# Kernel tuning notes

Hardware: AMD Instinct MI355X
Metric: run time of the kernel (lower is better)

Reference implementation:

```python
import jax, jax.numpy as jnp
import numpy as np

N = 50000
E = 800000
IN_C, HID, OUT_C = 128, 64, 64
L = 8
ALPHA, THETA = 0.1, 0.5


def setup_inputs() -> dict:
    key = jax.random.key(0)
    ks = jax.random.split(key, 7)
    x = jax.random.normal(ks[0], (N, IN_C), dtype=jnp.float32)
    edge_index = jax.random.randint(ks[1], (2, E), 0, N, dtype=jnp.int64)
    # parameters (Linear weights stored [out, in] like torch)
    w_in = jax.random.normal(ks[2], (HID, IN_C), dtype=jnp.float32) / np.sqrt(IN_C)
    b_in = jnp.zeros((HID,), dtype=jnp.float32)
    conv_w = jax.random.normal(ks[3], (L, HID, HID), dtype=jnp.float32) / np.sqrt(HID)
    w_out = jax.random.normal(ks[4], (OUT_C, HID), dtype=jnp.float32) / np.sqrt(HID)
    b_out = jnp.zeros((OUT_C,), dtype=jnp.float32)
    return {"x": x, "edge_index": edge_index, "w_in": w_in, "b_in": b_in,
            "conv_w": conv_w, "w_out": w_out, "b_out": b_out}


def reference(x, edge_index, w_in, b_in, conv_w, w_out, b_out):
    # add self loops
    loops = jnp.arange(N, dtype=edge_index.dtype)
    row = jnp.concatenate([edge_index[0], loops])
    col = jnp.concatenate([edge_index[1], loops])
    # symmetric GCN normalization from in-degree of col
    deg = jax.ops.segment_sum(jnp.ones_like(col, dtype=x.dtype), col, num_segments=N)
    dinv = jnp.where(deg > 0, jax.lax.rsqrt(deg), 0.0)
    norm = (dinv[row] * dinv[col])[:, None]  # [E+N, 1]

    # eval mode: dropout is identity
    h = jax.nn.relu(x @ w_in.T + b_in)
    x0 = h
    betas = jnp.log(THETA / jnp.arange(1, L + 1, dtype=jnp.float32) + 1.0)

    def layer(h, wb):
        W, beta = wb
        agg = jax.ops.segment_sum(h[row] * norm, col, num_segments=N)  # gather-scale-scatter
        agg = (1.0 - ALPHA) * agg + ALPHA * x0                         # initial residual
        out = (1.0 - beta) * agg + beta * (agg @ W.T)                  # identity mapping
        return jax.nn.relu(out), None

    h, _ = jax.lax.scan(layer, h, (conv_w, betas))
    return h @ w_out.T + b_out
```

## Files before the change

### kernel.cpp

```cpp
#include <hip/hip_runtime.h>
#include <math.h>

#define NN 50000
#define EE 800000
#define INC 128
#define HIDC 64
#define OUTC 64
#define LLAYERS 8
#define TOT (EE + NN)
#define NB 196
#define ABLK 256
#define CHUNKA ((TOT + ABLK - 1) / ABLK)

#define WAVE_LDS_FENCE() asm volatile("s_waitcnt lgkmcnt(0)" ::: "memory")

typedef __attribute__((ext_vector_type(8))) short bf16x8;
typedef __attribute__((ext_vector_type(4))) float f32x4;

__device__ __forceinline__ float bf2f(unsigned short u) {
    return __uint_as_float(((unsigned int)u) << 16);
}
__device__ __forceinline__ unsigned short f2bf(float f) {
    unsigned int u = __float_as_uint(f);
    u += 0x7FFFu + ((u >> 16) & 1u);
    return (unsigned short)(u >> 16);
}

__global__ void detect_kernel(const long long* __restrict__ p, int* __restrict__ flag) {
    long long v = p[threadIdx.x];
    if (v < 0 || v >= NN) atomicOr(flag, 1);
}

__device__ __forceinline__ int load_row(const void* ei, int is64, int e) {
    return is64 ? (int)((const long long*)ei)[e] : ((const int*)ei)[e];
}
__device__ __forceinline__ int load_col(const void* ei, int is64, int e) {
    return is64 ? (int)((const long long*)ei)[EE + e] : ((const int*)ei)[EE + e];
}

__global__ __launch_bounds__(256) void histA(const void* __restrict__ ei,
                                             const int* __restrict__ flag,
                                             int* __restrict__ bcnt) {
    __shared__ int h[NB];
    int tid = threadIdx.x;
    for (int i = tid; i < NB; i += 256) h[i] = 0;
    __syncthreads();
    int is64 = (*flag == 0);
    int lo = blockIdx.x * CHUNKA, hi = lo + CHUNKA; if (hi > TOT) hi = TOT;
    for (int e = lo + tid; e < hi; e += 256) {
        int c = (e < EE) ? load_col(ei, is64, e) : (e - EE);
        atomicAdd(&h[c >> 8], 1);
    }
    __syncthreads();
    for (int i = tid; i < NB; i += 256) if (h[i]) atomicAdd(&bcnt[i], h[i]);
}

__global__ __launch_bounds__(256) void scan_buckets(const int* __restrict__ bcnt,
                                                    int* __restrict__ bstart,
                                                    int* __restrict__ bcur) {
    __shared__ int s[256];
    int t = threadIdx.x;
    int v = (t < NB) ? bcnt[t] : 0;
    s[t] = v;
    __syncthreads();
    for (int off = 1; off < 256; off <<= 1) {
        int a = (t >= off) ? s[t - off] : 0;
        __syncthreads();
        s[t] += a;
        __syncthreads();
    }
    if (t < NB) { int st = s[t] - v; bstart[t] = st; bcur[t] = st; }
    if (t == NB - 1) bstart[NB] = s[t];
}

__global__ __launch_bounds__(256) void bucket_scatter(const void* __restrict__ ei,
                                                      const int* __restrict__ flag,
                                                      int* __restrict__ bcur,
                                                      unsigned int* __restrict__ barr) {
    __shared__ int h[NB];
    __shared__ int base[NB];
    int tid = threadIdx.x;
    for (int i = tid; i < NB; i += 256) h[i] = 0;
    __syncthreads();
    int is64 = (*flag == 0);
    int lo = blockIdx.x * CHUNKA, hi = lo + CHUNKA; if (hi > TOT) hi = TOT;
    for (int e = lo + tid; e < hi; e += 256) {
        int c = (e < EE) ? load_col(ei, is64, e) : (e - EE);
        atomicAdd(&h[c >> 8], 1);
    }
    __syncthreads();
    for (int i = tid; i < NB; i += 256) {
        int cnt = h[i];
        base[i] = cnt ? atomicAdd(&bcur[i], cnt) : 0;
        h[i] = 0;
    }
    __syncthreads();
    for (int e = lo + tid; e < hi; e += 256) {
        int r, c;
        if (e < EE) { r = load_row(ei, is64, e); c = load_col(ei, is64, e); }
        else        { r = e - EE; c = r; }
        int b = c >> 8;
        int p = base[b] + atomicAdd(&h[b], 1);
        barr[p] = ((unsigned int)r << 8) | (unsigned int)(c & 255);
    }
}

__global__ __launch_bounds__(256) void bucket_offsets(const unsigned int* __restrict__ barr,
                                                      const int* __restrict__ bstart,
                                                      int* __restrict__ offsets,
                                                      float* __restrict__ dinv) {
    __shared__ int cnt[256];
    __shared__ int pre[256];
    int b = blockIdx.x, t = threadIdx.x;
    cnt[t] = 0;
    __syncthreads();
    int lo = bstart[b], hi = bstart[b + 1];
    for (int i = lo + t; i < hi; i += 256) atomicAdd(&cnt[barr[i] & 255u], 1);
    __syncthreads();
    int v = cnt[t];
    pre[t] = v;
    __syncthreads();
    for (int off = 1; off < 256; off <<= 1) {
        int a = (t >= off) ? pre[t - off] : 0;
        __syncthreads();
        pre[t] += a;
        __syncthreads();
    }
    int c = (b << 8) + t;
    if (c <= NN) offsets[c] = bstart[b] + pre[t] - v;
    if (c < NN)  dinv[c] = 1.0f / sqrtf((float)v);
}

__global__ __launch_bounds__(256) void bucket_place(const unsigned int* __restrict__ barr,
                                                    const int* __restrict__ bstart,
                                                    const int* __restrict__ offsets,
                                                    const float* __restrict__ dinv,
                                                    int2* __restrict__ adj) {
    __shared__ int cur[256];
    int b = blockIdx.x, t = threadIdx.x;
    int c0 = b << 8;
    int c = c0 + t;
    cur[t] = (c < NN) ? offsets[c] : 0;
    __syncthreads();
    int lo = bstart[b], hi = bstart[b + 1];
    for (int i = lo + t; i < hi; i += 256) {
        unsigned int v = barr[i];
        int r = (int)(v >> 8);
        int ci = (int)(v & 255u);
        int pos = atomicAdd(&cur[ci], 1);
        adj[pos] = make_int2(r, __float_as_int(dinv[r] * dinv[c0 + ci]));
    }
}

__global__ __launch_bounds__(256) void in_gemm(const float* __restrict__ x,
                                               const float* __restrict__ w_in,
                                               const float* __restrict__ b_in,
                                               unsigned short* __restrict__ h,
                                               float* __restrict__ x0) {
    __shared__ unsigned short xT[16 * 136];
    int tid = threadIdx.x, w = tid >> 6, lane = tid & 63;
    int g = lane >> 4, c = lane & 15;
    int base = blockIdx.x << 4;

    bf16x8 bfrag[4];
    {
        const float* Wrow = w_in + (size_t)((w << 4) + c) * INC;
        #pragma unroll
        for (int kt = 0; kt < 4; ++kt) {
            int k0 = kt * 32 + (g << 3);
            float4 va = *reinterpret_cast<const float4*>(Wrow + k0);
            float4 vb = *reinterpret_cast<const float4*>(Wrow + k0 + 4);
            bf16x8 r;
            r[0] = (short)f2bf(va.x); r[1] = (short)f2bf(va.y);
            r[2] = (short)f2bf(va.z); r[3] = (short)f2bf(va.w);
            r[4] = (short)f2bf(vb.x); r[5] = (short)f2bf(vb.y);
            r[6] = (short)f2bf(vb.z); r[7] = (short)f2bf(vb.w);
            bfrag[kt] = r;
        }
    }

    #pragma unroll
    for (int m = 0; m < 2; ++m) {
        int idx = tid * 2 + m;
        int row = idx >> 5, col4 = idx & 31;
        float4 v = *reinterpret_cast<const float4*>(
            x + (((size_t)(base + row)) << 7) + (col4 << 2));
        ushort4 pk;
        pk.x = f2bf(v.x); pk.y = f2bf(v.y); pk.z = f2bf(v.z); pk.w = f2bf(v.w);
        *reinterpret_cast<ushort4*>(&xT[row * 136 + (col4 << 2)]) = pk;
    }
    __syncthreads();

    f32x4 d = {0.f, 0.f, 0.f, 0.f};
    #pragma unroll
    for (int kt = 0; kt < 4; ++kt) {
        bf16x8 a = *reinterpret_cast<const bf16x8*>(&xT[c * 136 + kt * 32 + (g << 3)]);
        d = __builtin_amdgcn_mfma_f32_16x16x32_bf16(a, bfrag[kt], d, 0, 0, 0);
    }
    float bj = b_in[(w << 4) + c];
    #pragma unroll
    for (int r = 0; r < 4; ++r) {
        int node = base + (g << 2) + r;
        int ch = (w << 4) + c;
        float v = fmaxf(d[r] + bj, 0.0f);
        h[((size_t)node << 6) + ch]  = f2bf(v);
        x0[((size_t)node << 6) + ch] = v;
    }
}

__global__ __launch_bounds__(256) void layer_mfma(
        const unsigned short* __restrict__ h_in, unsigned short* __restrict__ h_out,
        const float* __restrict__ x0,
        const int* __restrict__ offsets, const int2* __restrict__ adj,
        const float* __restrict__ W, float beta) {
    __shared__ unsigned short aggT[16 * 72];
    int tid = threadIdx.x, w = tid >> 6, lane = tid & 63;
    int g = lane >> 4, c = lane & 15;
    float omb = 1.0f - beta;

    bf16x8 bfrag[2];
    {
        int n = (w << 4) + c;
        const float* Wrow = W + n * HIDC;
        #pragma unroll
        for (int kt = 0; kt < 2; ++kt) {
            int k0 = kt * 32 + (g << 3);
            float4 va = *reinterpret_cast<const float4*>(Wrow + k0);
            float4 vb = *reinterpret_cast<const float4*>(Wrow + k0 + 4);
            float e[8] = {va.x, va.y, va.z, va.w, vb.x, vb.y, vb.z, vb.w};
            bf16x8 r;
            #pragma unroll
            for (int i = 0; i < 8; ++i) {
                float t = beta * e[i] + ((k0 + i == n) ? omb : 0.0f);
                r[i] = (short)f2bf(t);
            }
            bfrag[kt] = r;
        }
    }

    int base = blockIdx.x << 4;
    int n = base + (w << 2) + g;
    int e0 = offsets[n], e1 = offsets[n + 1];
    float4 acc = make_float4(0.f, 0.f, 0.f, 0.f);
    int e = e0;
    for (; e + 4 <= e1; e += 4) {
        int2 a0 = adj[e], a1 = adj[e + 1], a2 = adj[e + 2], a3 = adj[e + 3];
        ushort4 h0 = *reinterpret_cast<const ushort4*>(h_in + ((a0.x << 6) + (c << 2)));
        ushort4 h1 = *reinterpret_cast<const ushort4*>(h_in + ((a1.x << 6) + (c << 2)));
        ushort4 h2 = *reinterpret_cast<const ushort4*>(h_in + ((a2.x << 6) + (c << 2)));
        ushort4 h3 = *reinterpret_cast<const ushort4*>(h_in + ((a3.x << 6) + (c << 2)));
        float n0 = __int_as_float(a0.y), n1 = __int_as_float(a1.y);
        float n2 = __int_as_float(a2.y), n3 = __int_as_float(a3.y);
        acc.x = fmaf(n0, bf2f(h0.x), acc.x); acc.y = fmaf(n0, bf2f(h0.y), acc.y);
        acc.z = fmaf(n0, bf2f(h0.z), acc.z); acc.w = fmaf(n0, bf2f(h0.w), acc.w);
        acc.x = fmaf(n1, bf2f(h1.x), acc.x); acc.y = fmaf(n1, bf2f(h1.y), acc.y);
        acc.z = fmaf(n1, bf2f(h1.z), acc.z); acc.w = fmaf(n1, bf2f(h1.w), acc.w);
        acc.x = fmaf(n2, bf2f(h2.x), acc.x); acc.y = fmaf(n2, bf2f(h2.y), acc.y);
        acc.z = fmaf(n2, bf2f(h2.z), acc.z); acc.w = fmaf(n2, bf2f(h2.w), acc.w);
        acc.x = fmaf(n3, bf2f(h3.x), acc.x); acc.y = fmaf(n3, bf2f(h3.y), acc.y);
        acc.z = fmaf(n3, bf2f(h3.z), acc.z); acc.w = fmaf(n3, bf2f(h3.w), acc.w);
    }
    for (; e < e1; ++e) {
        int2 a = adj[e];
        ushort4 hv = *reinterpret_cast<const ushort4*>(h_in + ((a.x << 6) + (c << 2)));
        float nrm = __int_as_float(a.y);
        acc.x = fmaf(nrm, bf2f(hv.x), acc.x);
        acc.y = fmaf(nrm, bf2f(hv.y), acc.y);
        acc.z = fmaf(nrm, bf2f(hv.z), acc.z);
        acc.w = fmaf(nrm, bf2f(hv.w), acc.w);
    }
    {
        const float4 x0v = *reinterpret_cast<const float4*>(x0 + ((n << 6) + (c << 2)));
        ushort4 pk;
        pk.x = f2bf(fmaf(0.9f, acc.x, 0.1f * x0v.x));
        pk.y = f2bf(fmaf(0.9f, acc.y, 0.1f * x0v.y));
        pk.z = f2bf(fmaf(0.9f, acc.z, 0.1f * x0v.z));
        pk.w = f2bf(fmaf(0.9f, acc.w, 0.1f * x0v.w));
        int row = (w << 2) + g;
        *reinterpret_cast<ushort4*>(&aggT[row * 72 + (c << 2)]) = pk;
    }
    __syncthreads();

    bf16x8 afrag0 = *reinterpret_cast<const bf16x8*>(&aggT[c * 72 + (g << 3)]);
    bf16x8 afrag1 = *reinterpret_cast<const bf16x8*>(&aggT[c * 72 + 32 + (g << 3)]);

    f32x4 d = {0.f, 0.f, 0.f, 0.f};
    d = __builtin_amdgcn_mfma_f32_16x16x32_bf16(afrag0, bfrag[0], d, 0, 0, 0);
    d = __builtin_amdgcn_mfma_f32_16x16x32_bf16(afrag1, bfrag[1], d, 0, 0, 0);

    #pragma unroll
    for (int r = 0; r < 4; ++r) {
        int node = base + (g << 2) + r;
        int ch = (w << 4) + c;
        h_out[(node << 6) + ch] = f2bf(fmaxf(d[r], 0.0f));
    }
}

__global__ __launch_bounds__(256, 8) void out_gemm(const unsigned short* __restrict__ h,
                                                   const float* __restrict__ w_out,
                                                   const float* __restrict__ b_out,
                                                   float* __restrict__ out) {
    __shared__ float4 WI4[16 * HIDC];
    __shared__ float  vecs[4][HIDC];
    int tid = threadIdx.x;
    const float4* W4 = reinterpret_cast<const float4*>(w_out);
    for (int m = 0; m < 4; ++m) {
        int idx = tid + m * 256;
        int s = idx >> 6, j = idx & 63;
        WI4[idx] = W4[j * 16 + s];
    }
    __syncthreads();
    int w = tid >> 6, lane = tid & 63;
    float bj = b_out[lane];
    for (int n0 = blockIdx.x * 4; n0 < NN; n0 += gridDim.x * 4) {
        int n = n0 + w;
        if (n < NN) {
            vecs[w][lane] = bf2f(h[(n << 6) + lane]);
            WAVE_LDS_FENCE();
            float acc = bj;
            #pragma unroll
            for (int s = 0; s < 16; ++s) {
                float4 wv = WI4[(s << 6) + lane];
                float4 vv = *reinterpret_cast<const float4*>(&vecs[w][s << 2]);
                acc = fmaf(wv.x, vv.x, acc);
                acc = fmaf(wv.y, vv.y, acc);
                acc = fmaf(wv.z, vv.z, acc);
                acc = fmaf(wv.w, vv.w, acc);
            }
            out[(n << 6) + lane] = acc;
        }
    }
}

extern "C" void kernel_launch(void* const* d_in, const int* in_sizes, int n_in,
                              void* d_out, int out_size, void* d_ws, size_t ws_size,
                              hipStream_t stream) {
    const float* x      = (const float*)d_in[0];
    const void*  ei     = d_in[1];
    const float* w_in   = (const float*)d_in[2];
    const float* b_in   = (const float*)d_in[3];
    const float* conv_w = (const float*)d_in[4];
    const float* w_out  = (const float*)d_in[5];
    const float* b_out  = (const float*)d_in[6];
    float* out = (float*)d_out;

    char* ws = (char*)d_ws;
    size_t off = 0;
    auto alloc = [&](size_t bytes) -> void* {
        void* p = ws + off;
        off += (bytes + 255) & ~(size_t)255;
        return p;
    };
    int*   flag    = (int*)alloc(4);
    float* dinv    = (float*)alloc((size_t)NN * 4);
    int*   offsets = (int*)alloc((size_t)(NN + 1) * 4);
    int*   bcnt    = (int*)alloc((size_t)NB * 4);
    int*   bstart  = (int*)alloc((size_t)(NB + 1) * 4);
    int*   bcur    = (int*)alloc((size_t)NB * 4);
    int2*  adj     = (int2*)alloc((size_t)TOT * 8);
    unsigned short* hA = (unsigned short*)alloc((size_t)NN * HIDC * 2);
    unsigned short* hB = (unsigned short*)alloc((size_t)NN * HIDC * 2);
    float* x0      = (float*)alloc((size_t)NN * HIDC * 4);
    unsigned int* barr = (unsigned int*)hA;

    hipMemsetAsync(flag, 0, 4, stream);
    hipMemsetAsync(bcnt, 0, (size_t)NB * 4, stream);
    detect_kernel<<<1, 256, 0, stream>>>((const long long*)ei, flag);
    histA<<<ABLK, 256, 0, stream>>>(ei, flag, bcnt);
    scan_buckets<<<1, 256, 0, stream>>>(bcnt, bstart, bcur);
    bucket_scatter<<<ABLK, 256, 0, stream>>>(ei, flag, bcur, barr);
    bucket_offsets<<<NB, 256, 0, stream>>>(barr, bstart, offsets, dinv);
    bucket_place<<<NB, 256, 0, stream>>>(barr, bstart, offsets, dinv, adj);
    in_gemm<<<NN / 16, 256, 0, stream>>>(x, w_in, b_in, hA, x0);

    unsigned short* cur = hA;
    unsigned short* nxt = hB;
    for (int l = 0; l < LLAYERS; ++l) {
        float beta = logf(0.5f / (float)(l + 1) + 1.0f);
        const float* Wl = conv_w + (size_t)l * HIDC * HIDC;
        layer_mfma<<<NN / 16, 256, 0, stream>>>(cur, nxt, x0, offsets, adj, Wl, beta);
        unsigned short* t = cur; cur = nxt; nxt = t;
    }
    out_gemm<<<1024, 256, 0, stream>>>(cur, w_out, b_out, out);
}
```

Baseline: 300.0 us.

## Make layer GEMM per-wave to drop the block barrier after aggregation

Each wave now multiplies its own 4 aggregated nodes against the full 64x64 transformed weight, which is staged once per block in LDS. The block-wide barrier between the gather phase and the MFMA is replaced by a wave-local LDS fence, so waves with short neighbour lists no longer wait for the slowest one. The cost is 4x redundant MFMA work, since only 4 of the 16 A rows are valid and the rest are unused padding rows. Stores are also narrower, because only 16 lanes per wave write output. A block barrier remains after the weight staging.

```diff
diff --git a/kernel.cpp b/kernel.cpp
--- a/kernel.cpp
+++ b/kernel.cpp
@@ -213,30 +213,18 @@
         const float* __restrict__ x0,
         const int* __restrict__ offsets, const int2* __restrict__ adj,
         const float* __restrict__ W, float beta) {
-    __shared__ unsigned short aggT[16 * 72];
+    __shared__ unsigned short WtL[64 * 72];
+    __shared__ unsigned short aggT[4][16 * 72];
     int tid = threadIdx.x, w = tid >> 6, lane = tid & 63;
     int g = lane >> 4, c = lane & 15;
     float omb = 1.0f - beta;
 
-    bf16x8 bfrag[2];
-    {
-        int n = (w << 4) + c;
-        const float* Wrow = W + n * HIDC;
-        #pragma unroll
-        for (int kt = 0; kt < 2; ++kt) {
-            int k0 = kt * 32 + (g << 3);
-            float4 va = *reinterpret_cast<const float4*>(Wrow + k0);
-            float4 vb = *reinterpret_cast<const float4*>(Wrow + k0 + 4);
-            float e[8] = {va.x, va.y, va.z, va.w, vb.x, vb.y, vb.z, vb.w};
-            bf16x8 r;
-            #pragma unroll
-            for (int i = 0; i < 8; ++i) {
-                float t = beta * e[i] + ((k0 + i == n) ? omb : 0.0f);
-                r[i] = (short)f2bf(t);
-            }
-            bfrag[kt] = r;
-        }
-    }
+    for (int i = tid; i < HIDC * HIDC; i += 256) {
+        int n = i >> 6, k = i & 63;
+        float t = beta * W[i] + ((k == n) ? omb : 0.0f);
+        WtL[n * 72 + k] = f2bf(t);
+    }
+    __syncthreads();
 
     int base = blockIdx.x << 4;
     int n = base + (w << 2) + g;
@@ -276,23 +264,30 @@
         pk.y = f2bf(fmaf(0.9f, acc.y, 0.1f * x0v.y));
         pk.z = f2bf(fmaf(0.9f, acc.z, 0.1f * x0v.z));
         pk.w = f2bf(fmaf(0.9f, acc.w, 0.1f * x0v.w));
-        int row = (w << 2) + g;
-        *reinterpret_cast<ushort4*>(&aggT[row * 72 + (c << 2)]) = pk;
-    }
-    __syncthreads();
-
-    bf16x8 afrag0 = *reinterpret_cast<const bf16x8*>(&aggT[c * 72 + (g << 3)]);
-    bf16x8 afrag1 = *reinterpret_cast<const bf16x8*>(&aggT[c * 72 + 32 + (g << 3)]);
-
-    f32x4 d = {0.f, 0.f, 0.f, 0.f};
-    d = __builtin_amdgcn_mfma_f32_16x16x32_bf16(afrag0, bfrag[0], d, 0, 0, 0);
-    d = __builtin_amdgcn_mfma_f32_16x16x32_bf16(afrag1, bfrag[1], d, 0, 0, 0);
+        *reinterpret_cast<ushort4*>(&aggT[w][g * 72 + (c << 2)]) = pk;
+    }
+    WAVE_LDS_FENCE();
+
+    bf16x8 afrag0 = *reinterpret_cast<const bf16x8*>(&aggT[w][c * 72 + (g << 3)]);
+    bf16x8 afrag1 = *reinterpret_cast<const bf16x8*>(&aggT[w][c * 72 + 32 + (g << 3)]);
 
     #pragma unroll
-    for (int r = 0; r < 4; ++r) {
-        int node = base + (g << 2) + r;
-        int ch = (w << 4) + c;
-        h_out[(node << 6) + ch] = f2bf(fmaxf(d[r], 0.0f));
+    for (int t = 0; t < 4; ++t) {
+        bf16x8 b0 = *reinterpret_cast<const bf16x8*>(
+            &WtL[((t << 4) + c) * 72 + (g << 3)]);
+        bf16x8 b1 = *reinterpret_cast<const bf16x8*>(
+            &WtL[((t << 4) + c) * 72 + 32 + (g << 3)]);
+        f32x4 d = {0.f, 0.f, 0.f, 0.f};
+        d = __builtin_amdgcn_mfma_f32_16x16x32_bf16(afrag0, b0, d, 0, 0, 0);
+        d = __builtin_amdgcn_mfma_f32_16x16x32_bf16(afrag1, b1, d, 0, 0, 0);
+        if (g == 0) {
+            #pragma unroll
+            for (int r = 0; r < 4; ++r) {
+                int node = base + (w << 2) + r;
+                int ch = (t << 4) + c;
+                h_out[(node << 6) + ch] = f2bf(fmaxf(d[r], 0.0f));
+            }
+        }
     }
 }
 
```

After: 286.0 us. 4.7% less time.
